# Optimization experiments

Measured on AMD Instinct MI355X. Metric: run time of the kernel, lower is better.

Reference implementation:

```python
import jax, jax.numpy as jnp
import numpy as np

N = 30          # num_nodes
F = 4           # feature_dim
H = 64          # decoder_hidden_dim
TF = 2          # decoder_tf_interval
MIN_VAR = 1e-8
MAX_VAR = 100.0

_pairs = np.array([(i, j) for i in range(N) for j in range(N) if i != j])
RECV = jnp.asarray(_pairs[:, 0])   # [E] receiver node per edge
SEND = jnp.asarray(_pairs[:, 1])   # [E] sender node per edge


def _mlp(x, Ws, bs, softplus=False):
    # Linear->ReLU for all hidden layers, final Linear; optional softplus+clip head
    for W, b in zip(Ws[:-1], bs[:-1]):
        x = jax.nn.relu(x @ W + b)
    x = x @ Ws[-1] + bs[-1]
    if softplus:
        x = jnp.clip(jax.nn.softplus(x), MIN_VAR, MAX_VAR)
    return x


def setup_inputs() -> dict:
    key = jax.random.key(0)
    ks = jax.random.split(key, 20)
    B, S, T = 8, 4, 128
    E = N * (N - 1)

    def lin(k, din, dout):
        s = 1.0 / np.sqrt(din)
        return jax.random.uniform(k, (din, dout), jnp.float32, -s, s)

    inp = {
        'data': jax.random.normal(ks[0], (B, S, T, N, F), jnp.float32),
        'graph': (jax.random.uniform(ks[1], (B * S, E)) > 0.5).astype(jnp.float32),
        # msg_fc: 2F -> H -> H
        'msg_W1': lin(ks[2], 2 * F, H), 'msg_b1': jnp.zeros((H,), jnp.float32),
        'msg_W2': lin(ks[3], H, H),     'msg_b2': jnp.zeros((H,), jnp.float32),
        # mean_fc: H -> H -> H -> F
        'mean_W1': lin(ks[4], H, H), 'mean_b1': jnp.zeros((H,), jnp.float32),
        'mean_W2': lin(ks[5], H, H), 'mean_b2': jnp.zeros((H,), jnp.float32),
        'mean_W3': lin(ks[6], H, F), 'mean_b3': jnp.zeros((F,), jnp.float32),
        # variance_fc: H -> H -> H -> F (softplus + clip)
        'var_W1': lin(ks[7], H, H), 'var_b1': jnp.zeros((H,), jnp.float32),
        'var_W2': lin(ks[8], H, H), 'var_b2': jnp.zeros((H,), jnp.float32),
        'var_W3': lin(ks[9], H, F), 'var_b3': jnp.zeros((F,), jnp.float32),
    }
    return inp


def _single_step(prev, graph, p):
    # prev: [B, C, N, F]; graph: [B, E]
    edge_hidden = jnp.concatenate([prev[:, :, RECV, :], prev[:, :, SEND, :]], axis=-1)  # [B,C,E,2F]
    msg = _mlp(edge_hidden, [p['msg_W1'], p['msg_W2']], [p['msg_b1'], p['msg_b2']])     # [B,C,E,H]
    msg = msg * graph[:, None, :, None]
    B, C = prev.shape[0], prev.shape[1]
    # edge2node: sum messages into receiver nodes (normalize=False)
    agg = jnp.zeros((B, C, N, msg.shape[-1]), msg.dtype).at[:, :, RECV, :].add(msg)     # [B,C,N,H]
    mu = _mlp(agg, [p['mean_W1'], p['mean_W2'], p['mean_W3']],
              [p['mean_b1'], p['mean_b2'], p['mean_b3']])
    var = _mlp(agg, [p['var_W1'], p['var_W2'], p['var_W3']],
               [p['var_b1'], p['var_b2'], p['var_b3']], softplus=True)
    return mu, var


def reference(data, graph, msg_W1, msg_b1, msg_W2, msg_b2,
              mean_W1, mean_b1, mean_W2, mean_b2, mean_W3, mean_b3,
              var_W1, var_b1, var_W2, var_b2, var_W3, var_b3):
    p = dict(msg_W1=msg_W1, msg_b1=msg_b1, msg_W2=msg_W2, msg_b2=msg_b2,
             mean_W1=mean_W1, mean_b1=mean_b1, mean_W2=mean_W2, mean_b2=mean_b2,
             mean_W3=mean_W3, mean_b3=mean_b3,
             var_W1=var_W1, var_b1=var_b1, var_W2=var_W2, var_b2=var_b2,
             var_W3=var_W3, var_b3=var_b3)
    B, S, T, Nn, Ff = data.shape
    x = data.reshape(B * S, T, Nn, Ff)
    prev = x[:, ::TF]                       # teacher-forced anchors, [B*S, C, N, F]
    C = prev.shape[1]
    mus, vars = [], []
    for _ in range(TF):
        mu, var = _single_step(prev, graph, p)
        mus.append(mu)
        vars.append(var)
        prev = mu
    # interleave: out[:, i::TF] = step_i
    mu_pred = jnp.stack(mus, axis=2).reshape(B * S, C * TF, Nn, Ff)[:, :T - 1]
    var_pred = jnp.stack(vars, axis=2).reshape(B * S, C * TF, Nn, Ff)[:, :T - 1]
    mu_pred = mu_pred.reshape(B, S, T - 1, Nn, Ff)
    var_pred = var_pred.reshape(B, S, T - 1, Nn, Ff)
    return mu_pred, var_pred
```

## Files before the change

kernel.cpp:

```cpp
#include <hip/hip_runtime.h>
#include <hip/hip_bf16.h>

typedef unsigned short u16;
typedef unsigned int u32;
typedef __attribute__((ext_vector_type(4))) short short4v;
typedef __attribute__((ext_vector_type(4))) float f32x4;

#define NN 30
#define FF 4
#define EE 870
#define BSZ 32
#define CC 64
#define TT 128
#define NF 120
#define TSTRIDE 15240
#define OUTHALF 487680
#define AST 68
#define WST 68
#define NCPB 2
#define BPB  16

#define WS_WOFF 256
#define WS_MASKOFF (256 + 45056)

__device__ __forceinline__ float bf2f(u16 u) {
    union { u32 i; float f; } v; v.i = ((u32)u) << 16; return v.f;
}
__device__ __forceinline__ u16 f2bf(float f) {
    __hip_bfloat16 h = __float2bfloat16(f); return *(u16*)&h;
}
__device__ __forceinline__ float ldv(const void* p, int idx, int isbf) {
    if (isbf) return bf2f(((const u16*)p)[idx]);
    return ((const float*)p)[idx];
}
__device__ __forceinline__ float softplus_clip(float z) {
    float sp = fmaxf(z, 0.f) + log1pf(expf(-fabsf(z)));
    return fminf(fmaxf(sp, 1e-8f), 100.f);
}
__device__ __forceinline__ f32x4 MFMA16(short4v a, short4v b, f32x4 c) {
    return __builtin_amdgcn_mfma_f32_16x16x16bf16_1k(a, b, c, 0, 0, 0);
}

__device__ __forceinline__ int probe_isbf(const u16* g, int lane) {
    int hit = (g[2 * lane] == 0x3F80u) | (g[128 + 2 * lane] == 0x3F80u);
    unsigned long long b = __ballot(hit);
    return (b != 0ull) ? 1 : 0;
}

__global__ void prep_ws(const void* __restrict__ mW2,
                        const void* __restrict__ aW1, const void* __restrict__ aW2,
                        const void* __restrict__ vW1, const void* __restrict__ vW2,
                        const void* __restrict__ graph,
                        u16* __restrict__ wsW, u32* __restrict__ wsMask) {
    const int lane = threadIdx.x & 63;
    const int isbf = probe_isbf((const u16*)graph, lane);
    const int gtid = blockIdx.x * blockDim.x + threadIdx.x;
    const int gstr = gridDim.x * blockDim.x;
    for (int idx = gtid; idx < 4096; idx += gstr) {
        int k = idx >> 6, o = idx & 63;
        int d = o * 64 + k;
        wsW[d]         = f2bf(ldv(mW2, idx, isbf));
        wsW[4096 + d]  = f2bf(ldv(aW1, idx, isbf));
        wsW[8192 + d]  = f2bf(ldv(aW2, idx, isbf));
        wsW[12288 + d] = f2bf(ldv(vW1, idx, isbf));
        wsW[16384 + d] = f2bf(ldv(vW2, idx, isbf));
    }
    for (int idx = gtid; idx < BSZ * NN; idx += gstr) {
        int b = idx / NN, i = idx % NN;
        u32 m = 0;
        for (int e = 0; e < 29; e++)
            if (ldv(graph, b * EE + i * 29 + e, isbf) > 0.5f) m |= (1u << e);
        wsMask[idx] = m;
    }
}

__global__ __launch_bounds__(512, 4)
void sim_fused(const void* __restrict__ data,
               const void* __restrict__ graph,
               const void* __restrict__ mW1, const void* __restrict__ mB1,
               const void* __restrict__ mB2,
               const void* __restrict__ aB1, const void* __restrict__ aB2,
               const void* __restrict__ aB3,
               const void* __restrict__ vB1, const void* __restrict__ vB2,
               const void* __restrict__ vB3,
               const void* __restrict__ aW3, const void* __restrict__ vW3,
               const u16* __restrict__ wsW, const u32* __restrict__ wsMask,
               void* __restrict__ out)
{
    __shared__ __align__(16) float xN[2][NF];
    __shared__ __align__(16) u16 pJs[2][NN * 64];
    __shared__ __align__(16) u32 gmaskS[32];
    __shared__ __align__(16) u16 S[2][32 * AST];
    __shared__ __align__(16) u16 lwM2[64 * WST];
    __shared__ __align__(16) u16 lwH1m[64 * WST];
    __shared__ __align__(16) u16 lwH2m[64 * WST];
    __shared__ __align__(16) u16 lwH1v[64 * WST];
    __shared__ __align__(16) u16 lwH2v[64 * WST];
    __shared__ __align__(16) float biasL[5 * 64];

    const int tid  = threadIdx.x;
    const int lane = tid & 63;
    const int wv   = tid >> 6;
    const int set  = wv >> 2;
    const int swv  = wv & 3;
    const int ln15 = lane & 15;
    const int quad = lane >> 4;
    const int bs   = blockIdx.x / BPB;
    const int bg   = blockIdx.x % BPB;
    const int cg   = bg * 2 + set;
    const int isbf = probe_isbf((const u16*)graph, lane);

    const bool isMean = (swv < 2);
    const int nb = swv & 1;

    {
        const u32* w32 = (const u32*)wsW;
        for (int idx = tid; idx < 2048; idx += 512) {
            int o = idx >> 5, kw = idx & 31;
            int d = o * (WST / 2) + kw;
            ((u32*)lwM2)[d]  = w32[idx];
            ((u32*)lwH1m)[d] = w32[2048 + idx];
            ((u32*)lwH2m)[d] = w32[4096 + idx];
            ((u32*)lwH1v)[d] = w32[6144 + idx];
            ((u32*)lwH2v)[d] = w32[8192 + idx];
        }
    }
    if (tid < 64) {
        biasL[tid]       = ldv(mB2, tid, isbf);
        biasL[64 + tid]  = ldv(aB1, tid, isbf);
        biasL[128 + tid] = ldv(aB2, tid, isbf);
        biasL[192 + tid] = ldv(vB1, tid, isbf);
        biasL[256 + tid] = ldv(vB2, tid, isbf);
    }
    if (tid < 32) gmaskS[tid] = (tid < NN) ? wsMask[bs * NN + tid] : 0u;
    if (tid < 256) {
        int s2 = tid >> 7, row = 30 + ((tid >> 6) & 1);
        S[s2][row * AST + (tid & 63)] = 0;
    }

    float w1r[8];
#pragma unroll
    for (int k = 0; k < 8; k++) w1r[k] = ldv(mW1, k * 64 + lane, isbf);
    const float b1r = ldv(mB1, lane, isbf);
    float b3r[4];
#pragma unroll
    for (int r = 0; r < 4; r++) b3r[r] = ldv(isMean ? aB3 : vB3, r, isbf);

    const u16* wH1 = isMean ? lwH1m : lwH1v;
    const u16* wH2 = isMean ? lwH2m : lwH2v;
    const float* bAgg = biasL;
    const float* bH1  = isMean ? (biasL + 64)  : (biasL + 192);
    const float* bH2  = isMean ? (biasL + 128) : (biasL + 256);

    const void* W3src = isMean ? aW3 : vW3;
    short4v eA[4];
#pragma unroll
    for (int kb = 0; kb < 4; kb++) {
        union { short4v v; u16 s[4]; } pk;
#pragma unroll
        for (int j = 0; j < 4; j++) {
            int k = kb * 16 + quad * 4 + j;
            pk.s[j] = (ln15 < 4)
                ? (isbf ? ((const u16*)W3src)[k * 4 + ln15]
                        : f2bf(((const float*)W3src)[k * 4 + ln15]))
                : (u16)0;
        }
        eA[kb] = pk.v;
    }

    __syncthreads();

    const int myNode = nb * 16 + ln15;
    const float ngp = (myNode < NN) ? (float)__popc(gmaskS[myNode]) : 0.f;

    auto runLayer = [&](const u16* wl, const float* bl, const short4v* Bin,
                        short4v* Bout, float bscale, bool doRelu) {
#pragma unroll
        for (int fb = 0; fb < 4; fb++) {
            f32x4 acc = {0.f, 0.f, 0.f, 0.f};
#pragma unroll
            for (int kb = 0; kb < 4; kb++) {
                short4v a = *(const short4v*)&wl[(fb * 16 + ln15) * WST + kb * 16 + quad * 4];
                acc = MFMA16(a, Bin[kb], acc);
            }
            float4 bv = *(const float4*)&bl[fb * 16 + quad * 4];
            union { short4v v; u16 s[4]; } pk;
#pragma unroll
            for (int r = 0; r < 4; r++) {
                float val = acc[r] + bscale * (&bv.x)[r];
                if (doRelu) val = fmaxf(val, 0.f);
                pk.s[r] = f2bf(val);
            }
            Bout[fb] = pk.v;
        }
    };

    const int setTid = tid & 255;

    for (int ci = 0; ci < NCPB; ci++) {
        const int c = cg * NCPB + ci;

        if (isbf) {
            if (setTid < 60) {
                u32 w = ((const u32*)data)[((bs * TT + 2 * c) * NF) / 2 + setTid];
                xN[set][setTid * 2]     = bf2f((u16)(w & 0xFFFF));
                xN[set][setTid * 2 + 1] = bf2f((u16)(w >> 16));
            }
        } else {
            if (setTid < NF) xN[set][setTid] = ((const float*)data)[(bs * TT + 2 * c) * NF + setTid];
        }
        __syncthreads();

        for (int step = 0; step < 2; step++) {
            for (int i = swv; i < NN; i += 4) {
                float4 xv = *(const float4*)&xN[set][i * 4];
                pJs[set][i * 64 + lane] =
                    f2bf(xv.x * w1r[4] + xv.y * w1r[5] + xv.z * w1r[6] + xv.w * w1r[7]);
            }
            __syncthreads();

            for (int i = swv; i < NN; i += 4) {
                float4 xv = *(const float4*)&xN[set][i * 4];
                float pI = b1r + xv.x * w1r[0] + xv.y * w1r[1] + xv.z * w1r[2] + xv.w * w1r[3];
                u32 gm = __builtin_amdgcn_readfirstlane(gmaskS[i]);
                float s = 0.f;
#pragma unroll
                for (int e = 0; e < 29; e++) {
                    if (gm & (1u << e)) {
                        int j = e + (e >= i);
                        s += fmaxf(pI + bf2f(pJs[set][j * 64 + lane]), 0.f);
                    }
                }
                S[set][i * AST + lane] = f2bf(s);
            }
            __syncthreads();

            short4v Bs[4], Ba[4], Bb[4];
#pragma unroll
            for (int kb = 0; kb < 4; kb++)
                Bs[kb] = *(const short4v*)&S[set][(nb * 16 + ln15) * AST + kb * 16 + quad * 4];

            runLayer(lwM2, bAgg, Bs, Ba, ngp, false);
            runLayer(wH1,  bH1,  Ba, Bb, 1.f, true);
            runLayer(wH2,  bH2,  Bb, Ba, 1.f, true);

            {
                f32x4 acc = {0.f, 0.f, 0.f, 0.f};
#pragma unroll
                for (int kb = 0; kb < 4; kb++) acc = MFMA16(eA[kb], Ba[kb], acc);
                const int n = nb * 16 + ln15;
                const int t = 2 * c + step;
                if (quad == 0 && n < NN) {
                    float v[4];
#pragma unroll
                    for (int r = 0; r < 4; r++) v[r] = acc[r] + b3r[r];
                    if (!isMean) {
#pragma unroll
                        for (int r = 0; r < 4; r++) v[r] = softplus_clip(v[r]);
                    }
                    if (t < 127) {
                        size_t o = (size_t)bs * TSTRIDE + (size_t)t * NF + n * 4
                                 + (isMean ? 0 : OUTHALF);
                        if (isbf) {
                            u16* op = (u16*)out;
                            u32 lo = (u32)f2bf(v[0]) | ((u32)f2bf(v[1]) << 16);
                            u32 hi = (u32)f2bf(v[2]) | ((u32)f2bf(v[3]) << 16);
                            *(u32*)&op[o] = lo;
                            *(u32*)&op[o + 2] = hi;
                        } else {
                            float* op = (float*)out;
                            op[o] = v[0]; op[o+1] = v[1]; op[o+2] = v[2]; op[o+3] = v[3];
                        }
                    }
                    if (isMean && step == 0) {
                        xN[set][n*4]   = v[0]; xN[set][n*4+1] = v[1];
                        xN[set][n*4+2] = v[2]; xN[set][n*4+3] = v[3];
                    }
                }
            }
            __syncthreads();
        }
    }
}

extern "C" void kernel_launch(void* const* d_in, const int* in_sizes, int n_in,
                              void* d_out, int out_size, void* d_ws, size_t ws_size,
                              hipStream_t stream) {
    (void)in_sizes; (void)n_in; (void)out_size; (void)ws_size;

    const void* data  = d_in[0];
    const void* graph = d_in[1];
    const void* mW1 = d_in[2];  const void* mB1 = d_in[3];
    const void* mW2 = d_in[4];  const void* mB2 = d_in[5];
    const void* aW1 = d_in[6];  const void* aB1 = d_in[7];
    const void* aW2 = d_in[8];  const void* aB2 = d_in[9];
    const void* aW3 = d_in[10]; const void* aB3 = d_in[11];
    const void* vW1 = d_in[12]; const void* vB1 = d_in[13];
    const void* vW2 = d_in[14]; const void* vB2 = d_in[15];
    const void* vW3 = d_in[16]; const void* vB3 = d_in[17];

    u16* wsW    = (u16*)((char*)d_ws + WS_WOFF);
    u32* wsMask = (u32*)((char*)d_ws + WS_MASKOFF);

    prep_ws<<<8, 256, 0, stream>>>(mW2, aW1, aW2, vW1, vW2,
                                   graph, wsW, wsMask);

    sim_fused<<<BSZ * BPB, 512, 0, stream>>>(data, graph,
        mW1, mB1, mB2, aB1, aB2, aB3, vB1, vB2, vB3,
        aW3, vW3, wsW, wsMask, d_out);
}
```

Baseline: 156.0 us.

## Keep sender projections in registers and give each wave set a single chunk

```diff
diff --git a/kernel.cpp b/kernel.cpp
--- a/kernel.cpp
+++ b/kernel.cpp
@@ -17,8 +17,6 @@
 #define OUTHALF 487680
 #define AST 68
 #define WST 68
-#define NCPB 2
-#define BPB  16
 
 #define WS_WOFF 256
 #define WS_MASKOFF (256 + 45056)
@@ -26,8 +24,18 @@
 __device__ __forceinline__ float bf2f(u16 u) {
     union { u32 i; float f; } v; v.i = ((u32)u) << 16; return v.f;
 }
+__device__ __forceinline__ float lo2f(u32 u) {
+    union { u32 i; float f; } v; v.i = u << 16; return v.f;
+}
+__device__ __forceinline__ float hi2f(u32 u) {
+    union { u32 i; float f; } v; v.i = u & 0xFFFF0000u; return v.f;
+}
 __device__ __forceinline__ u16 f2bf(float f) {
     __hip_bfloat16 h = __float2bfloat16(f); return *(u16*)&h;
+}
+__device__ __forceinline__ u16 f2bf_fast(float f) {
+    union { float f; u32 u; } v; v.f = f;
+    return (u16)((v.u + 0x7FFFu + ((v.u >> 16) & 1u)) >> 16);
 }
 __device__ __forceinline__ float ldv(const void* p, int idx, int isbf) {
     if (isbf) return bf2f(((const u16*)p)[idx]);
@@ -74,7 +82,7 @@
     }
 }
 
-__global__ __launch_bounds__(512, 4)
+__global__ __launch_bounds__(512, 6)
 void sim_fused(const void* __restrict__ data,
                const void* __restrict__ graph,
                const void* __restrict__ mW1, const void* __restrict__ mB1,
@@ -88,7 +96,6 @@
                void* __restrict__ out)
 {
     __shared__ __align__(16) float xN[2][NF];
-    __shared__ __align__(16) u16 pJs[2][NN * 64];
     __shared__ __align__(16) u32 gmaskS[32];
     __shared__ __align__(16) u16 S[2][32 * AST];
     __shared__ __align__(16) u16 lwM2[64 * WST];
@@ -96,7 +103,7 @@
     __shared__ __align__(16) u16 lwH2m[64 * WST];
     __shared__ __align__(16) u16 lwH1v[64 * WST];
     __shared__ __align__(16) u16 lwH2v[64 * WST];
-    __shared__ __align__(16) float biasL[5 * 64];
+    __shared__ __align__(16) u16 biasU[5 * 64];
 
     const int tid  = threadIdx.x;
     const int lane = tid & 63;
@@ -105,9 +112,9 @@
     const int swv  = wv & 3;
     const int ln15 = lane & 15;
     const int quad = lane >> 4;
-    const int bs   = blockIdx.x / BPB;
-    const int bg   = blockIdx.x % BPB;
-    const int cg   = bg * 2 + set;
+    const int bs   = blockIdx.x >> 5;
+    const int bg   = blockIdx.x & 31;
+    const int c    = (bg << 1) | set;
     const int isbf = probe_isbf((const u16*)graph, lane);
 
     const bool isMean = (swv < 2);
@@ -126,11 +133,11 @@
         }
     }
     if (tid < 64) {
-        biasL[tid]       = ldv(mB2, tid, isbf);
-        biasL[64 + tid]  = ldv(aB1, tid, isbf);
-        biasL[128 + tid] = ldv(aB2, tid, isbf);
-        biasL[192 + tid] = ldv(vB1, tid, isbf);
-        biasL[256 + tid] = ldv(vB2, tid, isbf);
+        biasU[tid]       = f2bf_fast(ldv(mB2, tid, isbf));
+        biasU[64 + tid]  = f2bf_fast(ldv(aB1, tid, isbf));
+        biasU[128 + tid] = f2bf_fast(ldv(aB2, tid, isbf));
+        biasU[192 + tid] = f2bf_fast(ldv(vB1, tid, isbf));
+        biasU[256 + tid] = f2bf_fast(ldv(vB2, tid, isbf));
     }
     if (tid < 32) gmaskS[tid] = (tid < NN) ? wsMask[bs * NN + tid] : 0u;
     if (tid < 256) {
@@ -148,9 +155,9 @@
 
     const u16* wH1 = isMean ? lwH1m : lwH1v;
     const u16* wH2 = isMean ? lwH2m : lwH2v;
-    const float* bAgg = biasL;
-    const float* bH1  = isMean ? (biasL + 64)  : (biasL + 192);
-    const float* bH2  = isMean ? (biasL + 128) : (biasL + 256);
+    const u16* bAgg = biasU;
+    const u16* bH1  = isMean ? (biasU + 64)  : (biasU + 192);
+    const u16* bH2  = isMean ? (biasU + 128) : (biasU + 256);
 
     const void* W3src = isMean ? aW3 : vW3;
     short4v eA[4];
@@ -168,12 +175,23 @@
         eA[kb] = pk.v;
     }
 
+    const int setTid = tid & 255;
+    if (isbf) {
+        if (setTid < 60) {
+            u32 w = ((const u32*)data)[((bs * TT + 2 * c) * NF) / 2 + setTid];
+            xN[set][setTid * 2]     = bf2f((u16)(w & 0xFFFF));
+            xN[set][setTid * 2 + 1] = bf2f((u16)(w >> 16));
+        }
+    } else {
+        if (setTid < NF) xN[set][setTid] = ((const float*)data)[(bs * TT + 2 * c) * NF + setTid];
+    }
+
     __syncthreads();
 
     const int myNode = nb * 16 + ln15;
     const float ngp = (myNode < NN) ? (float)__popc(gmaskS[myNode]) : 0.f;
 
-    auto runLayer = [&](const u16* wl, const float* bl, const short4v* Bin,
+    auto runLayer = [&](const u16* wl, const u16* bl, const short4v* Bin,
                         short4v* Bout, float bscale, bool doRelu) {
 #pragma unroll
         for (int fb = 0; fb < 4; fb++) {
@@ -183,103 +201,100 @@
                 short4v a = *(const short4v*)&wl[(fb * 16 + ln15) * WST + kb * 16 + quad * 4];
                 acc = MFMA16(a, Bin[kb], acc);
             }
-            float4 bv = *(const float4*)&bl[fb * 16 + quad * 4];
+            u32 b01 = *(const u32*)&bl[fb * 16 + quad * 4];
+            u32 b23 = *(const u32*)&bl[fb * 16 + quad * 4 + 2];
+            float bvs0 = lo2f(b01), bvs1 = hi2f(b01), bvs2 = lo2f(b23), bvs3 = hi2f(b23);
             union { short4v v; u16 s[4]; } pk;
-#pragma unroll
-            for (int r = 0; r < 4; r++) {
-                float val = acc[r] + bscale * (&bv.x)[r];
-                if (doRelu) val = fmaxf(val, 0.f);
-                pk.s[r] = f2bf(val);
+            float v0 = acc[0] + bscale * bvs0;
+            float v1 = acc[1] + bscale * bvs1;
+            float v2 = acc[2] + bscale * bvs2;
+            float v3 = acc[3] + bscale * bvs3;
+            if (doRelu) {
+                v0 = fmaxf(v0, 0.f); v1 = fmaxf(v1, 0.f);
+                v2 = fmaxf(v2, 0.f); v3 = fmaxf(v3, 0.f);
             }
+            pk.s[0] = f2bf_fast(v0); pk.s[1] = f2bf_fast(v1);
+            pk.s[2] = f2bf_fast(v2); pk.s[3] = f2bf_fast(v3);
             Bout[fb] = pk.v;
         }
     };
 
-    const int setTid = tid & 255;
-
-    for (int ci = 0; ci < NCPB; ci++) {
-        const int c = cg * NCPB + ci;
-
-        if (isbf) {
-            if (setTid < 60) {
-                u32 w = ((const u32*)data)[((bs * TT + 2 * c) * NF) / 2 + setTid];
-                xN[set][setTid * 2]     = bf2f((u16)(w & 0xFFFF));
-                xN[set][setTid * 2 + 1] = bf2f((u16)(w >> 16));
+    for (int step = 0; step < 2; step++) {
+        u32 pJp[15];
+#pragma unroll
+        for (int jp = 0; jp < 15; jp++) {
+            float4 x0 = *(const float4*)&xN[set][(2 * jp) * 4];
+            float4 x1 = *(const float4*)&xN[set][(2 * jp + 1) * 4];
+            float v0 = x0.x * w1r[4] + x0.y * w1r[5] + x0.z * w1r[6] + x0.w * w1r[7];
+            float v1 = x1.x * w1r[4] + x1.y * w1r[5] + x1.z * w1r[6] + x1.w * w1r[7];
+            pJp[jp] = (u32)f2bf_fast(v0) | ((u32)f2bf_fast(v1) << 16);
+        }
+
+        for (int i = swv; i < NN; i += 4) {
+            float4 xv = *(const float4*)&xN[set][i * 4];
+            float pI = b1r + xv.x * w1r[0] + xv.y * w1r[1] + xv.z * w1r[2] + xv.w * w1r[3];
+            u32 gm = __builtin_amdgcn_readfirstlane(gmaskS[i]);
+            u32 gmj = (gm & ((1u << i) - 1u)) | ((gm >> i) << (i + 1));
+            float s = 0.f;
+#pragma unroll
+            for (int jp = 0; jp < 15; jp++) {
+                if (gmj & (1u << (2 * jp))) {
+                    union { u32 u; float f; } t; t.u = pJp[jp] << 16;
+                    s += fmaxf(pI + t.f, 0.f);
+                }
+                if (gmj & (1u << (2 * jp + 1))) {
+                    union { u32 u; float f; } t; t.u = pJp[jp] & 0xFFFF0000u;
+                    s += fmaxf(pI + t.f, 0.f);
+                }
             }
-        } else {
-            if (setTid < NF) xN[set][setTid] = ((const float*)data)[(bs * TT + 2 * c) * NF + setTid];
+            S[set][i * AST + lane] = f2bf_fast(s);
         }
         __syncthreads();
 
-        for (int step = 0; step < 2; step++) {
-            for (int i = swv; i < NN; i += 4) {
-                float4 xv = *(const float4*)&xN[set][i * 4];
-                pJs[set][i * 64 + lane] =
-                    f2bf(xv.x * w1r[4] + xv.y * w1r[5] + xv.z * w1r[6] + xv.w * w1r[7]);
+        short4v Bs[4], Ba[4], Bb[4];
+#pragma unroll
+        for (int kb = 0; kb < 4; kb++)
+            Bs[kb] = *(const short4v*)&S[set][(nb * 16 + ln15) * AST + kb * 16 + quad * 4];
+
+        runLayer(lwM2, bAgg, Bs, Ba, ngp, false);
+        runLayer(wH1,  bH1,  Ba, Bb, 1.f, true);
+        runLayer(wH2,  bH2,  Bb, Ba, 1.f, true);
+
+        {
+            f32x4 acc = {0.f, 0.f, 0.f, 0.f};
+#pragma unroll
+            for (int kb = 0; kb < 4; kb++) acc = MFMA16(eA[kb], Ba[kb], acc);
+            const int n = nb * 16 + ln15;
+            const int t = 2 * c + step;
+            if (quad == 0 && n < NN) {
+                float v[4];
+#pragma unroll
+                for (int r = 0; r < 4; r++) v[r] = acc[r] + b3r[r];
+                if (!isMean) {
+#pragma unroll
+                    for (int r = 0; r < 4; r++) v[r] = softplus_clip(v[r]);
+                }
+                if (t < 127) {
+                    size_t o = (size_t)bs * TSTRIDE + (size_t)t * NF + n * 4
+                             + (isMean ? 0 : OUTHALF);
+                    if (isbf) {
+                        u16* op = (u16*)out;
+                        u32 lo = (u32)f2bf_fast(v[0]) | ((u32)f2bf_fast(v[1]) << 16);
+                        u32 hi = (u32)f2bf_fast(v[2]) | ((u32)f2bf_fast(v[3]) << 16);
+                        *(u32*)&op[o] = lo;
+                        *(u32*)&op[o + 2] = hi;
+                    } else {
+                        float* op = (float*)out;
+                        op[o] = v[0]; op[o+1] = v[1]; op[o+2] = v[2]; op[o+3] = v[3];
+                    }
+                }
+                if (isMean && step == 0) {
+                    xN[set][n*4]   = v[0]; xN[set][n*4+1] = v[1];
+                    xN[set][n*4+2] = v[2]; xN[set][n*4+3] = v[3];
+                }
             }
-            __syncthreads();
-
-            for (int i = swv; i < NN; i += 4) {
-                float4 xv = *(const float4*)&xN[set][i * 4];
-                float pI = b1r + xv.x * w1r[0] + xv.y * w1r[1] + xv.z * w1r[2] + xv.w * w1r[3];
-                u32 gm = __builtin_amdgcn_readfirstlane(gmaskS[i]);
-                float s = 0.f;
-#pragma unroll
-                for (int e = 0; e < 29; e++) {
-                    if (gm & (1u << e)) {
-                        int j = e + (e >= i);
-                        s += fmaxf(pI + bf2f(pJs[set][j * 64 + lane]), 0.f);
-                    }
-                }
-                S[set][i * AST + lane] = f2bf(s);
-            }
-            __syncthreads();
-
-            short4v Bs[4], Ba[4], Bb[4];
-#pragma unroll
-            for (int kb = 0; kb < 4; kb++)
-                Bs[kb] = *(const short4v*)&S[set][(nb * 16 + ln15) * AST + kb * 16 + quad * 4];
-
-            runLayer(lwM2, bAgg, Bs, Ba, ngp, false);
-            runLayer(wH1,  bH1,  Ba, Bb, 1.f, true);
-            runLayer(wH2,  bH2,  Bb, Ba, 1.f, true);
-
-            {
-                f32x4 acc = {0.f, 0.f, 0.f, 0.f};
-#pragma unroll
-                for (int kb = 0; kb < 4; kb++) acc = MFMA16(eA[kb], Ba[kb], acc);
-                const int n = nb * 16 + ln15;
-                const int t = 2 * c + step;
-                if (quad == 0 && n < NN) {
-                    float v[4];
-#pragma unroll
-                    for (int r = 0; r < 4; r++) v[r] = acc[r] + b3r[r];
-                    if (!isMean) {
-#pragma unroll
-                        for (int r = 0; r < 4; r++) v[r] = softplus_clip(v[r]);
-                    }
-                    if (t < 127) {
-                        size_t o = (size_t)bs * TSTRIDE + (size_t)t * NF + n * 4
-                                 + (isMean ? 0 : OUTHALF);
-                        if (isbf) {
-                            u16* op = (u16*)out;
-                            u32 lo = (u32)f2bf(v[0]) | ((u32)f2bf(v[1]) << 16);
-                            u32 hi = (u32)f2bf(v[2]) | ((u32)f2bf(v[3]) << 16);
-                            *(u32*)&op[o] = lo;
-                            *(u32*)&op[o + 2] = hi;
-                        } else {
-                            float* op = (float*)out;
-                            op[o] = v[0]; op[o+1] = v[1]; op[o+2] = v[2]; op[o+3] = v[3];
-                        }
-                    }
-                    if (isMean && step == 0) {
-                        xN[set][n*4]   = v[0]; xN[set][n*4+1] = v[1];
-                        xN[set][n*4+2] = v[2]; xN[set][n*4+3] = v[3];
-                    }
-                }
-            }
-            __syncthreads();
-        }
+        }
+        __syncthreads();
     }
 }
 
@@ -305,7 +320,7 @@
     prep_ws<<<8, 256, 0, stream>>>(mW2, aW1, aW2, vW1, vW2,
                                    graph, wsW, wsMask);
 
-    sim_fused<<<BSZ * BPB, 512, 0, stream>>>(data, graph,
+    sim_fused<<<BSZ * 32, 512, 0, stream>>>(data, graph,
         mW1, mB1, mB2, aB1, aB2, aB3, vB1, vB2, vB3,
         aW3, vW3, wsW, wsMask, d_out);
 }
```

Result: slower. 169.4 us (+8.6%).
